# Optimization experiments

Measured on AMD Instinct MI355X. Metric: run time of the kernel, lower is better.

The kernel has to match this reference:

```python
import jax, jax.numpy as jnp
import numpy as np

B, S, T = 32, 128, 64
V, E, H = 32000, 256, 512


def setup_inputs() -> dict:
    key = jax.random.key(0)
    ks = jax.random.split(key, 32)
    n = jax.random.normal

    def lin(k, fi, fo):
        kw, kb = jax.random.split(k)
        s = 1.0 / np.sqrt(fi)
        return (jax.random.uniform(kw, (fi, fo), jnp.float32, -s, s),
                jax.random.uniform(kb, (fo,), jnp.float32, -s, s))

    W_enc, b_enc = lin(ks[4], 2 * H, H)      # attention.enc_h_in
    W_prev, b_prev = lin(ks[5], H, H)        # attention.prev_s_in
    W_att, b_att = lin(ks[6], H, 1)          # attention.linear
    Wi_g, bi_g = lin(ks[7], E, 2 * H)        # cell.input_weights
    Wh_g, bh_g = lin(ks[8], H, 2 * H)        # cell.hidden_weights
    Wc_g, bc_g = lin(ks[9], 2 * H, 2 * H)    # cell.ctx_weights
    Wi, bi = lin(ks[10], E, H)               # cell.input_in
    Wh, bh = lin(ks[11], H, H)               # cell.hidden_in
    Wc, bc = lin(ks[12], 2 * H, H)           # cell.ctx_in
    W_out, b_out = lin(ks[13], H, V)         # dec2word

    return dict(
        content=n(ks[0], (B, H), jnp.float32),
        sentiment=n(ks[1], (B, H), jnp.float32),
        hiddens=n(ks[2], (B, S, 2 * H), jnp.float32),
        target=jax.random.randint(ks[3], (B, T), 0, V, jnp.int32),
        embed=n(ks[14], (V, E), jnp.float32) * 0.02,
        W_enc=W_enc, b_enc=b_enc, W_prev=W_prev, b_prev=b_prev,
        W_att=W_att, b_att=b_att,
        Wi_g=Wi_g, bi_g=bi_g, Wh_g=Wh_g, bh_g=bh_g, Wc_g=Wc_g, bc_g=bc_g,
        Wi=Wi, bi=bi, Wh=Wh, bh=bh, Wc=Wc, bc=bc,
        W_out=W_out, b_out=b_out,
    )


def reference(content, sentiment, hiddens, target, embed,
              W_enc, b_enc, W_prev, b_prev, W_att, b_att,
              Wi_g, bi_g, Wh_g, bh_g, Wc_g, bc_g,
              Wi, bi, Wh, bh, Wc, bc, W_out, b_out):
    tgt_emb = embed[target]                       # [B, T, E]
    enc_proj = hiddens @ W_enc + b_enc            # [B, S, H], timestep-invariant

    def step(prev_s, x_t):
        # additive attention
        q = prev_s @ W_prev + b_prev              # [B, H]
        h = jnp.tanh(enc_proj + q[:, None, :])    # [B, S, H]
        score = h @ W_att + b_att                 # [B, S, 1]
        alpha = jax.nn.softmax(score, axis=1)     # over source positions
        ctx = jnp.einsum('bsi,bsh->bh', alpha, hiddens)  # [B, 2H]
        # GRU-like cell (original uses only the first gate, as written)
        gates = x_t @ Wi_g + bi_g + prev_s @ Wh_g + bh_g + ctx @ Wc_g + bc_g
        reset_gate, _update_gate = jnp.split(gates, 2, axis=1)
        r = jax.nn.sigmoid(reset_gate)
        s_tilde = jnp.tanh(x_t @ Wi + bi + prev_s @ Wh + bh + ctx @ Wc + bc)
        new_s = (1.0 - r) * prev_s + r * s_tilde
        return new_s, new_s

    _, dec_h = jax.lax.scan(step, content, jnp.swapaxes(tgt_emb, 0, 1))
    dec_h = jnp.swapaxes(dec_h, 0, 1)             # [B, T, H]
    style_logits = sentiment @ W_out + b_out      # [B, V], same every step
    outputs = (dec_h @ W_out + b_out) + 0.5 * style_logits[:, None, :]
    return outputs                                # [B, T, V]
```

## Files before the change

kernel.cpp:

```cpp
#include <hip/hip_runtime.h>
#include <hip/hip_bf16.h>
#include <math.h>

#define NB 32
#define NS 128
#define NT 64
#define NV 32000
#define NE 256
#define NH 512

typedef short s16x8 __attribute__((ext_vector_type(8)));
typedef float f32x4 __attribute__((ext_vector_type(4)));

__device__ __forceinline__ unsigned short f2bf(float x) {
    union { float f; unsigned u; } v; v.f = x;
    unsigned r = v.u + 0x7FFFu + ((v.u >> 16) & 1u);
    return (unsigned short)(r >> 16);
}
__device__ __forceinline__ float bf2f(short h) {
    union { unsigned u; float f; } x;
    x.u = ((unsigned)(unsigned short)h) << 16;
    return x.f;
}

__device__ __forceinline__ void gbar(unsigned* c, int idx, unsigned nb) {
    __syncthreads();
    if (threadIdx.x == 0) {
        __hip_atomic_fetch_add(&c[idx], 1u, __ATOMIC_RELAXED, __HIP_MEMORY_SCOPE_AGENT);
        while (__hip_atomic_load(&c[idx], __ATOMIC_RELAXED, __HIP_MEMORY_SCOPE_AGENT) < nb)
            __builtin_amdgcn_s_sleep(1);
    }
    __syncthreads();
    asm volatile("" ::: "memory");
}

__global__ void build_wfrag_k(const float* __restrict__ Wp,
                              const float* __restrict__ Whg,
                              const float* __restrict__ Wh,
                              unsigned short* __restrict__ wfrag) {
    int blk = blockIdx.x;
    int lane = threadIdx.x;
    int ct = blk >> 4, kt = blk & 15;
    int c = ct * 16 + (lane & 15);
    int kb = kt * 32 + (lane >> 4) * 8;
    s16x8 v;
#pragma unroll
    for (int j = 0; j < 8; ++j) {
        int k = kb + j;
        float x;
        if (c < 512)       x = Wp[k * 512 + c];
        else if (c < 1024) x = Whg[k * 1024 + (c - 512)];
        else               x = Wh[k * 512 + (c - 1024)];
        v[j] = (short)f2bf(x);
    }
    ((s16x8*)wfrag)[blk * 64 + lane] = v;
}

template<int MODE>
__global__ __launch_bounds__(256, 2) void gemm_mfma(
    const float* __restrict__ Af, const unsigned short* __restrict__ Abf,
    const int* __restrict__ gidx,
    const float* __restrict__ B0, const float* __restrict__ B1, const float* __restrict__ B2,
    const float* __restrict__ e0, const float* __restrict__ e1, const float* __restrict__ e2,
    const float* __restrict__ e3, const float* __restrict__ e4, const float* __restrict__ e5,
    void* __restrict__ O0v, void* __restrict__ O1v, void* __restrict__ O2v)
{
    constexpr int M   = (MODE == 0) ? 4096 : 2048;
    constexpr int K   = (MODE == 0) ? 1024 : ((MODE == 1) ? 256 : 512);
    constexpr int LDA = (MODE == 0) ? 1024 : ((MODE == 1) ? 256 : 512);
    constexpr int MB  = M / 128;

    const int bm = blockIdx.x % MB, bn = blockIdx.x / MB;
    const int m0 = bm * 128, n0 = bn * 128;

    const float* Bp; int ldb, coff;
    if constexpr (MODE == 0) {
        int sub = n0 >> 9;
        Bp   = (sub == 0) ? B0 : (sub == 1) ? B1 : B2;
        ldb  = (sub == 1) ? 1024 : 512;
        coff = n0 & 511;
    } else if constexpr (MODE == 1) {
        if (n0 < 512) { Bp = B0; ldb = 1024; coff = n0; }
        else          { Bp = B1; ldb = 512;  coff = n0 - 512; }
    } else {
        Bp = B0; ldb = 32000; coff = n0;
    }

    __shared__ unsigned short As[128 * 40];
    __shared__ unsigned short Bs[128 * 40];

    const int tid = threadIdx.x, lane = tid & 63, w = tid >> 6;
    const int wr = w >> 1, wc = w & 1;
    const int k0f = (lane >> 4) * 8;
    const int rsel = lane & 15;

    f32x4 acc[4][4];
#pragma unroll
    for (int i = 0; i < 4; ++i)
#pragma unroll
        for (int j = 0; j < 4; ++j) { f32x4 z = {0.f, 0.f, 0.f, 0.f}; acc[i][j] = z; }

    for (int kt = 0; kt < K / 32; ++kt) {
        const int k0 = kt * 32;
        __syncthreads();
#pragma unroll
        for (int i = 0; i < 16; ++i) {
            int idx = tid + i * 256;
            int r = idx >> 5, k = idx & 31;
            unsigned short v;
            if constexpr (MODE == 2) {
                v = Abf[(size_t)(m0 + r) * LDA + k0 + k];
            } else if constexpr (MODE == 1) {
                int g = gidx[m0 + r];
                v = f2bf(Af[(size_t)g * 256 + k0 + k]);
            } else {
                v = f2bf(Af[(size_t)(m0 + r) * LDA + k0 + k]);
            }
            As[r * 40 + k] = v;
        }
#pragma unroll
        for (int i = 0; i < 16; ++i) {
            int idx = tid + i * 256;
            int k = idx >> 7, c = idx & 127;
            Bs[c * 40 + k] = f2bf(Bp[(size_t)(k0 + k) * ldb + coff + c]);
        }
        __syncthreads();

        s16x8 af[4], bf[4];
#pragma unroll
        for (int i = 0; i < 4; ++i)
            af[i] = *(const s16x8*)&As[(wr * 64 + i * 16 + rsel) * 40 + k0f];
#pragma unroll
        for (int j = 0; j < 4; ++j)
            bf[j] = *(const s16x8*)&Bs[(wc * 64 + j * 16 + rsel) * 40 + k0f];
#pragma unroll
        for (int i = 0; i < 4; ++i)
#pragma unroll
            for (int j = 0; j < 4; ++j)
                acc[i][j] = __builtin_amdgcn_mfma_f32_16x16x32_bf16(af[i], bf[j], acc[i][j], 0, 0, 0);
    }

    const int rg = (lane >> 4) * 4;
#pragma unroll
    for (int i = 0; i < 4; ++i)
#pragma unroll
        for (int j = 0; j < 4; ++j) {
            int row0 = m0 + wr * 64 + i * 16 + rg;
            int col  = n0 + wc * 64 + j * 16 + rsel;
            if constexpr (MODE == 0) {
                int sub = col >> 9;
                if (sub == 0) {
                    unsigned short* Ta = (unsigned short*)O0v;
#pragma unroll
                    for (int r = 0; r < 4; ++r)
                        Ta[(size_t)(row0 + r) * 512 + col] = f2bf(tanhf(acc[i][j][r] + e0[col]));
                } else {
                    int h = col & 511;
                    int bb = row0 >> 7, s0 = row0 & 127;
                    unsigned long long pk = 0;
#pragma unroll
                    for (int r = 0; r < 4; ++r)
                        pk |= (unsigned long long)f2bf(acc[i][j][r]) << (16 * r);
                    unsigned short* dstp = (sub == 1) ? (unsigned short*)O1v : (unsigned short*)O2v;
                    *(unsigned long long*)&dstp[(size_t)((bb * 512 + h) * 128 + s0)] = pk;
                }
            } else if constexpr (MODE == 1) {
                float* Of = (float*)O0v;
                float bias;
                if (col < 512) bias = e0[col] + e1[col] + e2[col];
                else { int h = col - 512; bias = e3[h] + e4[h] + e5[h]; }
#pragma unroll
                for (int r = 0; r < 4; ++r)
                    Of[(size_t)(row0 + r) * 1024 + col] = acc[i][j][r] + bias;
            } else {
                float* Of = (float*)O0v;
#pragma unroll
                for (int r = 0; r < 4; ++r)
                    Of[(size_t)(row0 + r) * 32000 + col] = acc[i][j][r] + 1.5f * e0[col];
            }
        }
}

__global__ __launch_bounds__(1024) void scan_coop(
    const float* __restrict__ content, const float* __restrict__ sentiment,
    const float* __restrict__ b_prev,  const float* __restrict__ W_att,
    const unsigned short* __restrict__ Ta_bf,
    const unsigned short* __restrict__ hWcg_t,
    const unsigned short* __restrict__ hWc_t,
    const float* __restrict__ xgxs, const unsigned short* __restrict__ wfrag,
    unsigned long long* __restrict__ S64, float* __restrict__ Ug,
    unsigned* __restrict__ ctr, unsigned short* __restrict__ dh)
{
    const int b = blockIdx.x;
    const int tid = threadIdx.x, lane = tid & 63, w = tid >> 6;

    __shared__ unsigned short W_lds[3 * 16 * 64 * 8];
    __shared__ unsigned short S_lds[32 * 512];
    __shared__ float tq[512];
    __shared__ float sc[128], al[128];
    __shared__ float s_f[512];
    __shared__ unsigned short s_b[512];
    __shared__ float cg[512], cs[512];

    {
        const s16x8* src = (const s16x8*)wfrag + (size_t)b * (3 * 16 * 64);
        s16x8* dst = (s16x8*)W_lds;
        for (int i = tid; i < 3 * 16 * 64; i += 1024) dst[i] = src[i];
    }
    float senth = 0.f, bprev_h = 0.f;
    if (tid < 512) {
        float v = content[b * 512 + tid];
        s_f[tid] = v;
        s_b[tid] = f2bf(v);
        senth = 0.5f * sentiment[b * 512 + tid];
        bprev_h = b_prev[tid];
    }
    float wv[8];
    {
        const f32x4* wa = (const f32x4*)&W_att[lane * 8];
        f32x4 a0 = wa[0], a1 = wa[1];
#pragma unroll
        for (int j = 0; j < 4; ++j) { wv[j] = a0[j]; wv[4 + j] = a1[j]; }
    }
    const int kbase = (lane >> 4) * 8;

    __syncthreads();
    if (tid < 128) {
        unsigned long long pk = *(const unsigned long long*)&s_b[tid * 4];
        __hip_atomic_store(&S64[b * 128 + tid], pk, __ATOMIC_RELAXED, __HIP_MEMORY_SCOPE_AGENT);
    }
    asm volatile("s_waitcnt vmcnt(0)" ::: "memory");
    gbar(ctr, 0, NB);

    for (int t = 0; t < 64; ++t) {
#pragma unroll
        for (int ii = 0; ii < 4; ++ii) {
            int i = tid + ii * 1024;
            unsigned long long pk = __hip_atomic_load(&S64[i], __ATOMIC_RELAXED, __HIP_MEMORY_SCOPE_AGENT);
            *(unsigned long long*)&S_lds[i * 4] = pk;
        }
        __syncthreads();
        if (w < 6) {
            const int mt = w & 1, ct = w >> 1;
            const int arow = mt * 16 + (lane & 15);
            f32x4 a4 = {0.f, 0.f, 0.f, 0.f};
            const s16x8* wl = (const s16x8*)W_lds;
#pragma unroll
            for (int kt = 0; kt < 16; ++kt) {
                s16x8 a = *(const s16x8*)&S_lds[arow * 512 + kt * 32 + kbase];
                s16x8 bfr = wl[(ct * 16 + kt) * 64 + lane];
                a4 = __builtin_amdgcn_mfma_f32_16x16x32_bf16(a, bfr, a4, 0, 0, 0);
            }
            const int cout = b * 48 + ct * 16 + (lane & 15);
            const int rbase = mt * 16 + (lane >> 4) * 4;
#pragma unroll
            for (int r = 0; r < 4; ++r)
                __hip_atomic_store(&Ug[(rbase + r) * 1536 + cout], a4[r],
                                   __ATOMIC_RELAXED, __HIP_MEMORY_SCOPE_AGENT);
        }
        asm volatile("s_waitcnt vmcnt(0)" ::: "memory");
        gbar(ctr, 1 + 2 * t, NB);

        float guv = 0.f, suv = 0.f;
        if (tid < 512) {
            float qv = __hip_atomic_load(&Ug[b * 1536 + tid],        __ATOMIC_RELAXED, __HIP_MEMORY_SCOPE_AGENT);
            guv      = __hip_atomic_load(&Ug[b * 1536 + 512 + tid],  __ATOMIC_RELAXED, __HIP_MEMORY_SCOPE_AGENT);
            suv      = __hip_atomic_load(&Ug[b * 1536 + 1024 + tid], __ATOMIC_RELAXED, __HIP_MEMORY_SCOPE_AGENT);
            tq[tid] = tanhf(qv + bprev_h);
        }
        __syncthreads();
        {
            float tqv[8];
            {
                const f32x4* tp = (const f32x4*)&tq[lane * 8];
                f32x4 t0 = tp[0], t1 = tp[1];
#pragma unroll
                for (int j = 0; j < 4; ++j) { tqv[j] = t0[j]; tqv[4 + j] = t1[j]; }
            }
#pragma unroll
            for (int s8 = 0; s8 < 8; ++s8) {
                int s = w * 8 + s8;
                s16x8 tv = *(const s16x8*)&Ta_bf[((size_t)(b * 128 + s)) * 512 + lane * 8];
                float a = 0.f;
#pragma unroll
                for (int j = 0; j < 8; ++j) {
                    float ta = bf2f(tv[j]);
                    float num = ta + tqv[j];
                    float den = fmaf(ta, tqv[j], 1.0f);
                    a = fmaf(wv[j], num * __builtin_amdgcn_rcpf(den), a);
                }
#pragma unroll
                for (int off = 32; off; off >>= 1) a += __shfl_xor(a, off, 64);
                if (lane == 0) sc[s] = a;
            }
        }
        __syncthreads();
        if (w == 0) {
            float v0 = sc[lane], v1 = sc[lane + 64];
            float m = fmaxf(v0, v1);
#pragma unroll
            for (int off = 32; off; off >>= 1) m = fmaxf(m, __shfl_xor(m, off, 64));
            float p0 = __expf(v0 - m), p1 = __expf(v1 - m);
            float sm = p0 + p1;
#pragma unroll
            for (int off = 32; off; off >>= 1) sm += __shfl_xor(sm, off, 64);
            float inv = __builtin_amdgcn_rcpf(sm);
            al[lane] = p0 * inv; al[lane + 64] = p1 * inv;
        }
        __syncthreads();
        {
            int mat = tid >> 9, h = tid & 511;
            const s16x8* Mp = (const s16x8*)((mat ? hWc_t : hWcg_t) + ((size_t)(b * 512 + h)) * 128);
            float a0 = 0.f, a1 = 0.f;
#pragma unroll
            for (int q = 0; q < 16; ++q) {
                s16x8 v = Mp[q];
#pragma unroll
                for (int j = 0; j < 8; j += 2) {
                    a0 = fmaf(al[q * 8 + j],     bf2f(v[j]),     a0);
                    a1 = fmaf(al[q * 8 + j + 1], bf2f(v[j + 1]), a1);
                }
            }
            if (mat) cs[h] = a0 + a1; else cg[h] = a0 + a1;
        }
        __syncthreads();
        if (tid < 512) {
            int h = tid;
            size_t row = (size_t)b * 64 + t;
            float g  = guv + xgxs[row * 1024 + h]       + cg[h];
            float r  = __builtin_amdgcn_rcpf(1.0f + __expf(-g));
            float sp = suv + xgxs[row * 1024 + 512 + h] + cs[h];
            float e  = __expf(2.0f * sp);
            float st = 1.0f - 2.0f * __builtin_amdgcn_rcpf(e + 1.0f);
            float sold = s_f[h];
            float ns = sold + r * (st - sold);
            s_f[h] = ns;
            s_b[h] = f2bf(ns);
            dh[row * 512 + h] = f2bf(ns + senth);
        }
        __syncthreads();
        if (t < 63) {
            if (tid < 128) {
                unsigned long long pk = *(const unsigned long long*)&s_b[tid * 4];
                __hip_atomic_store(&S64[b * 128 + tid], pk, __ATOMIC_RELAXED, __HIP_MEMORY_SCOPE_AGENT);
            }
            asm volatile("s_waitcnt vmcnt(0)" ::: "memory");
            gbar(ctr, 2 + 2 * t, NB);
        }
    }
}

extern "C" void kernel_launch(void* const* d_in, const int* in_sizes, int n_in,
                              void* d_out, int out_size, void* d_ws, size_t ws_size,
                              hipStream_t stream) {
    const float* content  = (const float*)d_in[0];
    const float* sentiment= (const float*)d_in[1];
    const float* hiddens  = (const float*)d_in[2];
    const int*   target   = (const int*)  d_in[3];
    const float* embed    = (const float*)d_in[4];
    const float* W_enc = (const float*)d_in[5];  const float* b_enc = (const float*)d_in[6];
    const float* W_prev= (const float*)d_in[7];  const float* b_prev= (const float*)d_in[8];
    const float* W_att = (const float*)d_in[9];
    const float* Wi_g  = (const float*)d_in[11]; const float* bi_g  = (const float*)d_in[12];
    const float* Wh_g  = (const float*)d_in[13]; const float* bh_g  = (const float*)d_in[14];
    const float* Wc_g  = (const float*)d_in[15]; const float* bc_g  = (const float*)d_in[16];
    const float* Wi    = (const float*)d_in[17]; const float* bi    = (const float*)d_in[18];
    const float* Wh    = (const float*)d_in[19]; const float* bh    = (const float*)d_in[20];
    const float* Wc    = (const float*)d_in[21]; const float* bc    = (const float*)d_in[22];
    const float* W_out = (const float*)d_in[23]; const float* b_out = (const float*)d_in[24];
    float* out = (float*)d_out;

    char* ws = (char*)d_ws;
    unsigned short* wfrag = (unsigned short*)ws;
    unsigned* ctr   = (unsigned*)(ws + 0x180000);
    float* Ug       = (float*)(ws + 0x180400);
    unsigned short* Ta_bf   = (unsigned short*)(ws + 0x1B0400);
    unsigned short* hWcg_t  = (unsigned short*)(ws + 0x5B0400);
    unsigned short* hWc_t   = (unsigned short*)(ws + 0x9B0400);
    float* xgxs     = (float*)(ws + 0xDB0400);
    unsigned short* dh      = (unsigned short*)(ws + 0x15B0400);
    unsigned long long* S64 = (unsigned long long*)(ws + 0x17B0400);

    hipMemsetAsync(ctr, 0, 1024, stream);

    build_wfrag_k<<<96 * 16, 64, 0, stream>>>(W_prev, Wh_g, Wh, wfrag);

    gemm_mfma<0><<<32 * 12, 256, 0, stream>>>(
        hiddens, nullptr, nullptr, W_enc, Wc_g, Wc,
        b_enc, nullptr, nullptr, nullptr, nullptr, nullptr,
        (void*)Ta_bf, (void*)hWcg_t, (void*)hWc_t);

    gemm_mfma<1><<<16 * 8, 256, 0, stream>>>(
        embed, nullptr, target, Wi_g, Wi, nullptr,
        bi_g, bh_g, bc_g, bi, bh, bc,
        (void*)xgxs, nullptr, nullptr);

    scan_coop<<<NB, 1024, 0, stream>>>(
        content, sentiment, b_prev, W_att, Ta_bf, hWcg_t, hWc_t,
        xgxs, wfrag, S64, Ug, ctr, dh);

    gemm_mfma<2><<<16 * 250, 256, 0, stream>>>(
        nullptr, dh, nullptr, W_out, nullptr, nullptr,
        b_out, nullptr, nullptr, nullptr, nullptr, nullptr,
        (void*)out, nullptr, nullptr);

    (void)in_sizes; (void)n_in; (void)out_size; (void)ws_size;
}
```

Measured before the change: 1.553 ms.

## Replace grid barriers with per-block sequence flags in recurrent scan

```diff
diff --git a/kernel.cpp b/kernel.cpp
--- a/kernel.cpp
+++ b/kernel.cpp
@@ -23,14 +23,14 @@
     return x.f;
 }
 
-__device__ __forceinline__ void gbar(unsigned* c, int idx, unsigned nb) {
-    __syncthreads();
-    if (threadIdx.x == 0) {
-        __hip_atomic_fetch_add(&c[idx], 1u, __ATOMIC_RELAXED, __HIP_MEMORY_SCOPE_AGENT);
-        while (__hip_atomic_load(&c[idx], __ATOMIC_RELAXED, __HIP_MEMORY_SCOPE_AGENT) < nb)
-            __builtin_amdgcn_s_sleep(1);
-    }
-    __syncthreads();
+__device__ __forceinline__ void wait_flags(unsigned* flags, unsigned seq) {
+    const int lane = threadIdx.x & 63;
+    for (;;) {
+        unsigned v = 0xFFFFFFFFu;
+        if (lane < 32)
+            v = __hip_atomic_load(&flags[lane * 16], __ATOMIC_RELAXED, __HIP_MEMORY_SCOPE_AGENT);
+        if (__all(v >= seq)) break;
+    }
     asm volatile("" ::: "memory");
 }
 
@@ -188,19 +188,23 @@
     const unsigned short* __restrict__ hWcg_t,
     const unsigned short* __restrict__ hWc_t,
     const float* __restrict__ xgxs, const unsigned short* __restrict__ wfrag,
-    unsigned long long* __restrict__ S64, float* __restrict__ Ug,
-    unsigned* __restrict__ ctr, unsigned short* __restrict__ dh)
+    unsigned* __restrict__ S32, float* __restrict__ Ug,
+    unsigned* __restrict__ flagS, unsigned* __restrict__ flagU,
+    unsigned short* __restrict__ dh)
 {
     const int b = blockIdx.x;
     const int tid = threadIdx.x, lane = tid & 63, w = tid >> 6;
+    const unsigned long long* S64 = (const unsigned long long*)S32;
 
     __shared__ unsigned short W_lds[3 * 16 * 64 * 8];
-    __shared__ unsigned short S_lds[32 * 512];
     __shared__ float tq[512];
     __shared__ float sc[128], al[128];
     __shared__ float s_f[512];
-    __shared__ unsigned short s_b[512];
     __shared__ float cg[512], cs[512];
+    __shared__ unsigned ctrA[64], ctrS[64];
+
+    if (tid < 64) ctrA[tid] = 0;
+    else if (tid < 128) ctrS[tid - 64] = 0;
 
     {
         const s16x8* src = (const s16x8*)wfrag + (size_t)b * (3 * 16 * 64);
@@ -211,7 +215,6 @@
     if (tid < 512) {
         float v = content[b * 512 + tid];
         s_f[tid] = v;
-        s_b[tid] = f2bf(v);
         senth = 0.5f * sentiment[b * 512 + tid];
         bprev_h = b_prev[tid];
     }
@@ -222,34 +225,55 @@
 #pragma unroll
         for (int j = 0; j < 4; ++j) { wv[j] = a0[j]; wv[4 + j] = a1[j]; }
     }
-    const int kbase = (lane >> 4) * 8;
-
     __syncthreads();
-    if (tid < 128) {
-        unsigned long long pk = *(const unsigned long long*)&s_b[tid * 4];
-        __hip_atomic_store(&S64[b * 128 + tid], pk, __ATOMIC_RELAXED, __HIP_MEMORY_SCOPE_AGENT);
-    }
-    asm volatile("s_waitcnt vmcnt(0)" ::: "memory");
-    gbar(ctr, 0, NB);
+
+    if (tid < 512) {
+        float ns = s_f[tid];
+        float nsn = __shfl_down(ns, 1, 64);
+        if (!(lane & 1)) {
+            unsigned p = (unsigned)f2bf(ns) | ((unsigned)f2bf(nsn) << 16);
+            __hip_atomic_store(&S32[b * 256 + (tid >> 1)], p, __ATOMIC_RELAXED, __HIP_MEMORY_SCOPE_AGENT);
+        }
+        asm volatile("s_waitcnt vmcnt(0)" ::: "memory");
+        if (lane == 0) atomicAdd(&ctrS[0], 1u);
+    }
+    if (w == 8 && lane == 0) {
+        while (__hip_atomic_load(&ctrS[0], __ATOMIC_RELAXED, __HIP_MEMORY_SCOPE_WORKGROUP) < 8) {}
+        __hip_atomic_store(&flagS[b * 16], 1u, __ATOMIC_RELAXED, __HIP_MEMORY_SCOPE_AGENT);
+    }
 
     for (int t = 0; t < 64; ++t) {
-#pragma unroll
-        for (int ii = 0; ii < 4; ++ii) {
-            int i = tid + ii * 1024;
-            unsigned long long pk = __hip_atomic_load(&S64[i], __ATOMIC_RELAXED, __HIP_MEMORY_SCOPE_AGENT);
-            *(unsigned long long*)&S_lds[i * 4] = pk;
-        }
-        __syncthreads();
         if (w < 6) {
+            wait_flags(flagS, (unsigned)(t + 1));
             const int mt = w & 1, ct = w >> 1;
             const int arow = mt * 16 + (lane & 15);
+            const int koff = (lane >> 4) * 2;
+            unsigned long long sa0[16], sa1[16];
+#pragma unroll
+            for (int kt = 0; kt < 8; ++kt) {
+                sa0[2 * kt]     = __hip_atomic_load(&S64[arow * 128 + kt * 8 + koff],     __ATOMIC_RELAXED, __HIP_MEMORY_SCOPE_AGENT);
+                sa0[2 * kt + 1] = __hip_atomic_load(&S64[arow * 128 + kt * 8 + koff + 1], __ATOMIC_RELAXED, __HIP_MEMORY_SCOPE_AGENT);
+            }
+#pragma unroll
+            for (int kt = 0; kt < 8; ++kt) {
+                sa1[2 * kt]     = __hip_atomic_load(&S64[arow * 128 + (kt + 8) * 8 + koff],     __ATOMIC_RELAXED, __HIP_MEMORY_SCOPE_AGENT);
+                sa1[2 * kt + 1] = __hip_atomic_load(&S64[arow * 128 + (kt + 8) * 8 + koff + 1], __ATOMIC_RELAXED, __HIP_MEMORY_SCOPE_AGENT);
+            }
             f32x4 a4 = {0.f, 0.f, 0.f, 0.f};
             const s16x8* wl = (const s16x8*)W_lds;
 #pragma unroll
-            for (int kt = 0; kt < 16; ++kt) {
-                s16x8 a = *(const s16x8*)&S_lds[arow * 512 + kt * 32 + kbase];
+            for (int kt = 0; kt < 8; ++kt) {
+                union { unsigned long long q[2]; s16x8 v; } u;
+                u.q[0] = sa0[2 * kt]; u.q[1] = sa0[2 * kt + 1];
                 s16x8 bfr = wl[(ct * 16 + kt) * 64 + lane];
-                a4 = __builtin_amdgcn_mfma_f32_16x16x32_bf16(a, bfr, a4, 0, 0, 0);
+                a4 = __builtin_amdgcn_mfma_f32_16x16x32_bf16(u.v, bfr, a4, 0, 0, 0);
+            }
+#pragma unroll
+            for (int kt = 0; kt < 8; ++kt) {
+                union { unsigned long long q[2]; s16x8 v; } u;
+                u.q[0] = sa1[2 * kt]; u.q[1] = sa1[2 * kt + 1];
+                s16x8 bfr = wl[(ct * 16 + kt + 8) * 64 + lane];
+                a4 = __builtin_amdgcn_mfma_f32_16x16x32_bf16(u.v, bfr, a4, 0, 0, 0);
             }
             const int cout = b * 48 + ct * 16 + (lane & 15);
             const int rbase = mt * 16 + (lane >> 4) * 4;
@@ -257,12 +281,17 @@
             for (int r = 0; r < 4; ++r)
                 __hip_atomic_store(&Ug[(rbase + r) * 1536 + cout], a4[r],
                                    __ATOMIC_RELAXED, __HIP_MEMORY_SCOPE_AGENT);
-        }
-        asm volatile("s_waitcnt vmcnt(0)" ::: "memory");
-        gbar(ctr, 1 + 2 * t, NB);
+            asm volatile("s_waitcnt vmcnt(0)" ::: "memory");
+            if (lane == 0) atomicAdd(&ctrA[t], 1u);
+        }
+        if (w == 6 && lane == 0) {
+            while (__hip_atomic_load(&ctrA[t], __ATOMIC_RELAXED, __HIP_MEMORY_SCOPE_WORKGROUP) < 6) {}
+            __hip_atomic_store(&flagU[b * 16], (unsigned)(t + 1), __ATOMIC_RELAXED, __HIP_MEMORY_SCOPE_AGENT);
+        }
 
         float guv = 0.f, suv = 0.f;
         if (tid < 512) {
+            wait_flags(flagU, (unsigned)(t + 1));
             float qv = __hip_atomic_load(&Ug[b * 1536 + tid],        __ATOMIC_RELAXED, __HIP_MEMORY_SCOPE_AGENT);
             guv      = __hip_atomic_load(&Ug[b * 1536 + 512 + tid],  __ATOMIC_RELAXED, __HIP_MEMORY_SCOPE_AGENT);
             suv      = __hip_atomic_load(&Ug[b * 1536 + 1024 + tid], __ATOMIC_RELAXED, __HIP_MEMORY_SCOPE_AGENT);
@@ -335,17 +364,20 @@
             float sold = s_f[h];
             float ns = sold + r * (st - sold);
             s_f[h] = ns;
-            s_b[h] = f2bf(ns);
             dh[row * 512 + h] = f2bf(ns + senth);
-        }
-        __syncthreads();
-        if (t < 63) {
-            if (tid < 128) {
-                unsigned long long pk = *(const unsigned long long*)&s_b[tid * 4];
-                __hip_atomic_store(&S64[b * 128 + tid], pk, __ATOMIC_RELAXED, __HIP_MEMORY_SCOPE_AGENT);
-            }
-            asm volatile("s_waitcnt vmcnt(0)" ::: "memory");
-            gbar(ctr, 2 + 2 * t, NB);
+            float nsn = __shfl_down(ns, 1, 64);
+            if (t < 63) {
+                if (!(lane & 1)) {
+                    unsigned p = (unsigned)f2bf(ns) | ((unsigned)f2bf(nsn) << 16);
+                    __hip_atomic_store(&S32[b * 256 + (tid >> 1)], p, __ATOMIC_RELAXED, __HIP_MEMORY_SCOPE_AGENT);
+                }
+                asm volatile("s_waitcnt vmcnt(0)" ::: "memory");
+                if (lane == 0) atomicAdd(&ctrS[t + 1], 1u);
+            }
+        }
+        if (t < 63 && w == 8 && lane == 0) {
+            while (__hip_atomic_load(&ctrS[t + 1], __ATOMIC_RELAXED, __HIP_MEMORY_SCOPE_WORKGROUP) < 8) {}
+            __hip_atomic_store(&flagS[b * 16], (unsigned)(t + 2), __ATOMIC_RELAXED, __HIP_MEMORY_SCOPE_AGENT);
         }
     }
 }
@@ -372,16 +404,17 @@
 
     char* ws = (char*)d_ws;
     unsigned short* wfrag = (unsigned short*)ws;
-    unsigned* ctr   = (unsigned*)(ws + 0x180000);
-    float* Ug       = (float*)(ws + 0x180400);
-    unsigned short* Ta_bf   = (unsigned short*)(ws + 0x1B0400);
-    unsigned short* hWcg_t  = (unsigned short*)(ws + 0x5B0400);
-    unsigned short* hWc_t   = (unsigned short*)(ws + 0x9B0400);
-    float* xgxs     = (float*)(ws + 0xDB0400);
-    unsigned short* dh      = (unsigned short*)(ws + 0x15B0400);
-    unsigned long long* S64 = (unsigned long long*)(ws + 0x17B0400);
-
-    hipMemsetAsync(ctr, 0, 1024, stream);
+    unsigned* flagS = (unsigned*)(ws + 0x180000);
+    unsigned* flagU = (unsigned*)(ws + 0x180800);
+    float* Ug       = (float*)(ws + 0x181000);
+    unsigned short* Ta_bf   = (unsigned short*)(ws + 0x1B1000);
+    unsigned short* hWcg_t  = (unsigned short*)(ws + 0x5B1000);
+    unsigned short* hWc_t   = (unsigned short*)(ws + 0x9B1000);
+    float* xgxs     = (float*)(ws + 0xDB1000);
+    unsigned short* dh      = (unsigned short*)(ws + 0x15B1000);
+    unsigned* S32   = (unsigned*)(ws + 0x17B1000);
+
+    hipMemsetAsync(ws + 0x180000, 0, 4096, stream);
 
     build_wfrag_k<<<96 * 16, 64, 0, stream>>>(W_prev, Wh_g, Wh, wfrag);
 
@@ -397,7 +430,7 @@
 
     scan_coop<<<NB, 1024, 0, stream>>>(
         content, sentiment, b_prev, W_att, Ta_bf, hWcg_t, hWc_t,
-        xgxs, wfrag, S64, Ug, ctr, dh);
+        xgxs, wfrag, S32, Ug, flagS, flagU, dh);
 
     gemm_mfma<2><<<16 * 250, 256, 0, stream>>>(
         nullptr, dh, nullptr, W_out, nullptr, nullptr,
```

After: 1.847 ms. 19.0% more time.
